# Kernel optimization log

Measured on AMD Instinct MI355X. Metric: run time of the kernel, lower is better.

The kernel has to match this reference:

```python
import jax, jax.numpy as jnp
import numpy as np

B, N, D = 4, 1024, 32      # clouds, points per cloud, feature dim
NW = 4                     # n_weights
THRESHOLD = 0.5
J = 3                      # wavelet scales (as in forward: J = 3)


def setup_inputs() -> dict:
    key = jax.random.key(0)
    k1, k2 = jax.random.split(key)
    point_clouds = jax.random.normal(k1, (B, N, D), dtype=jnp.float32)
    alphas = jax.random.uniform(k2, (NW, D), dtype=jnp.float32)
    sigma = jnp.float32(50.0)
    return {"point_clouds": point_clouds, "alphas": alphas, "sigma": sigma}


def reference(point_clouds, alphas, sigma):
    # X_nodes = pc * alpha_w for every (cloud p, weight w): [B, NW, N, D]
    X = point_clouds[:, None, :, :] * alphas[None, :, None, :]
    # compute_dist: ||xi||^2 + ||xj||^2 - 2 <xi, xj>  -> [B, NW, N, N]
    sq = jnp.sum(X * X, axis=-1)
    G = jnp.einsum('bwnd,bwmd->bwnm', X, X)
    Dm = sq[..., :, None] + sq[..., None, :] - 2.0 * G
    K = jnp.exp(-Dm / sigma)
    # threshold graph: keep kernel weight where K >= threshold (self-loops kept, K_ii = 1)
    A = (K >= THRESHOLD).astype(X.dtype)
    Wm = K * A
    deg = jnp.sum(Wm, axis=-1)  # >= 1 via self-loop
    # lazy random-walk diffusion operator P = 0.5 (I + D^{-1} W)
    P = 0.5 * (jnp.eye(N, dtype=X.dtype) + Wm / deg[..., None])
    # dyadic powers P^(2^j), j = 0..J
    powers = [P]
    for _ in range(J):
        powers.append(jnp.einsum('bwnm,bwmk->bwnk', powers[-1], powers[-1]))

    def apply(M, F):
        return jnp.einsum('bwnm,bwmd->bwnd', M, F)

    # first-order scattering |psi_j X| with psi_j = P^(2^(j)) - P^(2^(j+1))
    first = [jnp.abs(apply(powers[j] - powers[j + 1], X)) for j in range(J)]
    # second-order |psi_k |psi_j X|| for j < k
    second = [jnp.abs(apply(powers[k] - powers[k + 1], first[j]))
              for j in range(J) for k in range(j + 1, J)]
    feats = jnp.concatenate([X] + first + second, axis=-1)  # [B, NW, N, F0]
    pooled = jnp.mean(feats, axis=2)                        # mean pooling -> [B, NW, F0]
    # final view(B_pc, features * n_weights)
    return pooled.reshape(B, -1)
```

## Files before the change

### kernel.cpp

```cpp
#include <hip/hip_runtime.h>
#include <math.h>

#define NPTS 1024
#define DIM 32
#define NPAIR 16

typedef __attribute__((ext_vector_type(8))) short short8;
typedef __attribute__((ext_vector_type(4))) float f32x4;
typedef __attribute__((ext_vector_type(8))) unsigned short ushort8v;
typedef unsigned short u16;
typedef unsigned char u8;


__device__ __forceinline__ u16 bf16_rne(float v) {
    unsigned u = __float_as_uint(v);
    return (u16)((u + 0x7fffu + ((u >> 16) & 1u)) >> 16);
}
__device__ __forceinline__ float bf16_to_f32(u16 b) {
    return __uint_as_float(((unsigned)b) << 16);
}

__device__ __forceinline__ short8 unpack_w8(unsigned lo, unsigned hi) {
    short8 r;
#pragma unroll
    for (int j = 0; j < 4; j++) {
        float f0 = (float)((lo >> (8 * j)) & 0xffu);
        float f1 = (float)((hi >> (8 * j)) & 0xffu);
        r[j]     = (short)(__float_as_uint(f0) >> 16);
        r[j + 4] = (short)(__float_as_uint(f1) >> 16);
    }
    return r;
}

__global__ __launch_bounds__(256) void build_X(const float* __restrict__ pc,
                                               const float* __restrict__ alphas,
                                               float* __restrict__ X,
                                               float* __restrict__ sqX,
                                               float* __restrict__ deg,
                                               u16* __restrict__ hiT,
                                               u16* __restrict__ loT,
                                               float* __restrict__ poolP) {
    __shared__ float S[DIM][68];
    int pair = blockIdx.y, n0 = blockIdx.x * 64, tid = threadIdx.x;
    int b = pair >> 2, w = pair & 3;
    for (int e = tid; e < 512; e += 256) {
        int e4 = e * 4;
        int dn = e4 >> 5, dq = e4 & 31;
        float4 p = *(const float4*)&pc[((size_t)b * NPTS + n0 + dn) * DIM + dq];
        float4 al = *(const float4*)&alphas[w * DIM + dq];
        float4 x = make_float4(p.x * al.x, p.y * al.y, p.z * al.z, p.w * al.w);
        *(float4*)&X[((size_t)pair * NPTS + n0 + dn) * DIM + dq] = x;
        S[dq][dn] = x.x; S[dq + 1][dn] = x.y; S[dq + 2][dn] = x.z; S[dq + 3][dn] = x.w;
    }
    __syncthreads();
    if (tid < 64) {
        float s = 0.f;
#pragma unroll
        for (int d = 0; d < DIM; d++) { float v = S[d][tid]; s += v * v; }
        sqX[pair * NPTS + n0 + tid] = s;
        deg[pair * NPTS + n0 + tid] = 0.0f;
    }
    if (tid < 64) {
        int h = tid >> 5, d = tid & 31;
        float s = 0.f;
#pragma unroll
        for (int k = 0; k < 32; k++) s += S[d][h * 32 + k];
        poolP[(((size_t)0 * NPAIR + pair) * 32 + 2 * blockIdx.x + h) * 32 + d] = s;
    }
    for (int idx = tid; idx < DIM * 4; idx += 256) {
        int row = idx >> 2, nq = (idx & 3) * 16;
        ushort8v hv[2], lv[2];
#pragma unroll
        for (int i = 0; i < 16; i++) {
            float v = S[row][nq + i];
            u16 hb = bf16_rne(v);
            hv[i >> 3][i & 7] = hb;
            lv[i >> 3][i & 7] = bf16_rne(v - bf16_to_f32(hb));
        }
        int c0 = n0 + nq;
        int kt = c0 >> 5;
        int q0 = (c0 >> 3) & 3;
        int mm = row & 15;
        size_t base = ((((size_t)pair * 2 + (row >> 4)) * 32 + kt) << 9);
        *(ushort8v*)(hiT + base + (size_t)(q0 * 16 + mm) * 8)       = hv[0];
        *(ushort8v*)(hiT + base + (size_t)((q0 + 1) * 16 + mm) * 8) = hv[1];
        *(ushort8v*)(loT + base + (size_t)(q0 * 16 + mm) * 8)       = lv[0];
        *(ushort8v*)(loT + base + (size_t)((q0 + 1) * 16 + mm) * 8) = lv[1];
    }
}

__global__ __launch_bounds__(256, 4) void W_kernel(const float* __restrict__ X,
                                                   const float* __restrict__ sqX,
                                                   const float* __restrict__ sigp,
                                                   float* __restrict__ deg,
                                                   u8* __restrict__ W8) {
    int bid = blockIdx.x;
    int xcd = bid & 7, loc = bid >> 3;
    int pair = xcd * 2 + (loc & 1);
    int j0 = ((loc >> 1) & 3) * 256;
    int i0 = (loc >> 3) * 64;
    float rsig = -1.0f / (*sigp);
    const float* Xp = X + (size_t)pair * NPTS * DIM;

    __shared__ float XiT[DIM][68];
    __shared__ float XjT[DIM][68];
    __shared__ float sqjS[64];

    int tid = threadIdx.x;
    int cx = tid & 15, ry = tid >> 4;

    {
        int r = tid & 63, dgb = (tid >> 6) * 4;
#pragma unroll
        for (int p = 0; p < 2; p++) {
            int dg = dgb + p * 16;
            float4 v = *(const float4*)&Xp[(size_t)(i0 + r) * DIM + dg];
            XiT[dg][r] = v.x; XiT[dg + 1][r] = v.y; XiT[dg + 2][r] = v.z; XiT[dg + 3][r] = v.w;
        }
    }
    float sqi[4];
#pragma unroll
    for (int a = 0; a < 4; a++) sqi[a] = sqX[pair * NPTS + i0 + ry * 4 + a];

    float rs[4] = {0.f, 0.f, 0.f, 0.f};
#pragma unroll 1
    for (int jt = 0; jt < 256; jt += 64) {
        __syncthreads();
        {
            int r = tid & 63, dgb = (tid >> 6) * 4;
#pragma unroll
            for (int p = 0; p < 2; p++) {
                int dg = dgb + p * 16;
                float4 v = *(const float4*)&Xp[(size_t)(j0 + jt + r) * DIM + dg];
                XjT[dg][r] = v.x; XjT[dg + 1][r] = v.y; XjT[dg + 2][r] = v.z; XjT[dg + 3][r] = v.w;
            }
        }
        if (tid < 64) sqjS[tid] = sqX[pair * NPTS + j0 + jt + tid];
        __syncthreads();

        float dot[4][4] = {};
#pragma unroll
        for (int d = 0; d < DIM; d++) {
            float4 a = *(const float4*)&XiT[d][ry * 4];
            float4 b = *(const float4*)&XjT[d][cx * 4];
            dot[0][0] += a.x * b.x; dot[0][1] += a.x * b.y; dot[0][2] += a.x * b.z; dot[0][3] += a.x * b.w;
            dot[1][0] += a.y * b.x; dot[1][1] += a.y * b.y; dot[1][2] += a.y * b.z; dot[1][3] += a.y * b.w;
            dot[2][0] += a.z * b.x; dot[2][1] += a.z * b.y; dot[2][2] += a.z * b.z; dot[2][3] += a.z * b.w;
            dot[3][0] += a.w * b.x; dot[3][1] += a.w * b.y; dot[3][2] += a.w * b.z; dot[3][3] += a.w * b.w;
        }
#pragma unroll
        for (int a = 0; a < 4; a++) {
            int i = i0 + ry * 4 + a;
            int jb = j0 + jt + cx * 4;
            unsigned qw = 0;
#pragma unroll
            for (int bb = 0; bb < 4; bb++) {
                float Dm = sqi[a] + sqjS[cx * 4 + bb] - 2.0f * dot[a][bb];
                float K = __expf(Dm * rsig);
                float Wv = (K >= 0.5f) ? K : 0.0f;
                unsigned q = (unsigned)fmaf(Wv, 255.0f, 0.5f);
                rs[a] += (float)q;
                qw |= q << (8 * bb);
            }
            int kt = jb >> 5;
            int quad = (jb >> 3) & 3;
            int jj = jb & 7;
            size_t o = ((((size_t)pair * 64 + (i >> 4)) * 32 + kt) << 9)
                     + (size_t)(quad * 16 + (i & 15)) * 8 + jj;
            *(unsigned*)(W8 + o) = qw;
        }
    }
#pragma unroll
    for (int a = 0; a < 4; a++) {
        float s = rs[a];
        s += __shfl_xor(s, 1); s += __shfl_xor(s, 2);
        s += __shfl_xor(s, 4); s += __shfl_xor(s, 8);
        if (cx == 0) atomicAdd(&deg[pair * NPTS + i0 + ry * 4 + a], s);
    }
}

template <int DC>
__global__ __launch_bounds__(512, 4) void apply_fused(const u8* __restrict__ W8,
                                                      const u16* __restrict__ Yhi,
                                                      const u16* __restrict__ Ylo,
                                                      const float* __restrict__ deg,
                                                      const float* __restrict__ prevF,
                                                      int prevStride, int prevOff,
                                                      float* __restrict__ dstF,
                                                      int dstStride, int dstOff,
                                                      float* __restrict__ sliceF,
                                                      u16* __restrict__ hiT, u16* __restrict__ loT,
                                                      int tC0, int tCN) {
    constexpr int NT = DC / 16;
    constexpr int SP = DC + 4;
    __shared__ float S[4][32][SP];
    __shared__ float rdegS[32];
    int bid = blockIdx.x;
    int pair = (bid & 7) * 2 + ((bid >> 3) & 1);
    int r0 = (bid >> 4) * 32;
    int tid = threadIdx.x;
    int wv = tid >> 6, lane = tid & 63;
    int m = lane & 15, quad = lane >> 4;

    if (tid < 32) rdegS[tid] = 0.5f / deg[pair * NPTS + r0 + tid];

    int rt0 = (bid >> 4) * 2;
    const u8*  Wb  = W8  + ((((size_t)pair * 64 + rt0) * 32 + wv * 4) << 9) + (size_t)lane * 8;
    const u16* Ybh = Yhi + (((size_t)pair * NT * 32 + wv * 4) << 9) + (size_t)lane * 8;
    const u16* Ybl = Ylo + (((size_t)pair * NT * 32 + wv * 4) << 9) + (size_t)lane * 8;

    f32x4 acc[2][NT];
#pragma unroll
    for (int mt = 0; mt < 2; mt++)
#pragma unroll
        for (int nt = 0; nt < NT; nt++)
#pragma unroll
            for (int i = 0; i < 4; i++) acc[mt][nt][i] = 0.0f;

#pragma unroll 2
    for (int c = 0; c < 4; c++) {
        uint2 a0q = *(const uint2*)(Wb + ((size_t)c << 9));
        uint2 a1q = *(const uint2*)(Wb + ((size_t)(32 + c) << 9));
        short8 a0h = unpack_w8(a0q.x, a0q.y);
        short8 a1h = unpack_w8(a1q.x, a1q.y);
#pragma unroll
        for (int nt = 0; nt < NT; nt++) {
            short8 bh = *(const short8*)(Ybh + ((size_t)(nt * 32 + c) << 9));
            short8 bl = *(const short8*)(Ybl + ((size_t)(nt * 32 + c) << 9));
            acc[0][nt] = __builtin_amdgcn_mfma_f32_16x16x32_bf16(a0h, bh, acc[0][nt], 0, 0, 0);
            acc[0][nt] = __builtin_amdgcn_mfma_f32_16x16x32_bf16(a0h, bl, acc[0][nt], 0, 0, 0);
            acc[1][nt] = __builtin_amdgcn_mfma_f32_16x16x32_bf16(a1h, bh, acc[1][nt], 0, 0, 0);
            acc[1][nt] = __builtin_amdgcn_mfma_f32_16x16x32_bf16(a1h, bl, acc[1][nt], 0, 0, 0);
        }
    }

    if (wv < 4) {
#pragma unroll
        for (int mt = 0; mt < 2; mt++)
#pragma unroll
            for (int nt = 0; nt < NT; nt++)
#pragma unroll
                for (int i = 0; i < 4; i++)
                    S[wv][mt * 16 + quad * 4 + i][nt * 16 + m] = acc[mt][nt][i];
    }
    __syncthreads();
    if (wv >= 4) {
#pragma unroll
        for (int mt = 0; mt < 2; mt++)
#pragma unroll
            for (int nt = 0; nt < NT; nt++)
#pragma unroll
                for (int i = 0; i < 4; i++)
                    S[wv - 4][mt * 16 + quad * 4 + i][nt * 16 + m] += acc[mt][nt][i];
    }
    __syncthreads();

    constexpr int E2 = 32 * DC / 4;
    for (int e = tid; e < E2; e += 512) {
        int e4 = e * 4;
        int n = e4 / DC, d = e4 % DC;
        float4 s0 = *(const float4*)&S[0][n][d];
        float4 s1 = *(const float4*)&S[1][n][d];
        float4 s2 = *(const float4*)&S[2][n][d];
        float4 s3 = *(const float4*)&S[3][n][d];
        float4 pv = *(const float4*)&prevF[((size_t)pair * NPTS + r0 + n) * prevStride + prevOff + d];
        float r = rdegS[n];
        float4 o = make_float4(0.5f * pv.x + r * (s0.x + s1.x + s2.x + s3.x),
                               0.5f * pv.y + r * (s0.y + s1.y + s2.y + s3.y),
                               0.5f * pv.z + r * (s0.z + s1.z + s2.z + s3.z),
                               0.5f * pv.w + r * (s0.w + s1.w + s2.w + s3.w));
        *(float4*)&dstF[((size_t)pair * NPTS + r0 + n) * dstStride + dstOff + d] = o;
        if (sliceF && d >= 32 && d < 64)
            *(float4*)&sliceF[((size_t)pair * NPTS + r0 + n) * 32 + (d - 32)] = o;
        *(float4*)&S[0][n][d] = o;
    }
    __syncthreads();

    if (hiT) {
        int NFo = tCN >> 4;
        for (int e = tid; e < tCN * 4; e += 512) {
            int row = e >> 2, nq = (e & 3) * 8;
            ushort8v hv, lv;
#pragma unroll
            for (int j = 0; j < 8; j++) {
                float v = S[0][nq + j][tC0 + row];
                u16 hb = bf16_rne(v);
                hv[j] = hb;
                lv[j] = bf16_rne(v - bf16_to_f32(hb));
            }
            int c0 = r0 + nq;
            size_t o = ((((size_t)pair * NFo + (row >> 4)) * 32 + (c0 >> 5)) << 9)
                     + (size_t)((((c0 >> 3) & 3) * 16 + (row & 15))) * 8;
            *(ushort8v*)(hiT + o) = hv;
            *(ushort8v*)(loT + o) = lv;
        }
    }
}

template <int DC>
__global__ __launch_bounds__(512, 4) void apply_fused2(const u8* __restrict__ W8,
                                                       const u16* __restrict__ Yhi,
                                                       const u16* __restrict__ Ylo,
                                                       const float* __restrict__ deg,
                                                       const float* __restrict__ prevF,
                                                       int prevStride, int prevOff,
                                                       float* __restrict__ dstF,
                                                       int dstStride, int dstOff,
                                                       float* __restrict__ sliceF,
                                                       u16* __restrict__ hiT, u16* __restrict__ loT,
                                                       int tC0, int tCN) {
    constexpr int NF = DC / 16;
    constexpr int SP = 36;
    __shared__ float S[4][64][SP];
    __shared__ float rdegS[64];
    int bid = blockIdx.x;
    int pair = (bid & 7) * 2 + ((bid >> 3) & 1);
    int rseg = (bid >> 4) & 15;
    int ch = bid >> 8;
    int r0 = rseg * 64;
    int tid = threadIdx.x;
    int wv = tid >> 6, lane = tid & 63;
    int m = lane & 15, quad = lane >> 4;

    if (tid < 64) rdegS[tid] = 0.5f / deg[pair * NPTS + r0 + tid];

    const u8*  Wb  = W8  + ((((size_t)pair * 64 + rseg * 4) * 32 + wv * 4) << 9) + (size_t)lane * 8;
    const u16* Ybh = Yhi + ((((size_t)pair * NF + ch * 2) * 32 + wv * 4) << 9) + (size_t)lane * 8;
    const u16* Ybl = Ylo + ((((size_t)pair * NF + ch * 2) * 32 + wv * 4) << 9) + (size_t)lane * 8;

    f32x4 acc[4][2];
#pragma unroll
    for (int mt = 0; mt < 4; mt++)
#pragma unroll
        for (int nt = 0; nt < 2; nt++)
#pragma unroll
            for (int i = 0; i < 4; i++) acc[mt][nt][i] = 0.0f;

#pragma unroll 2
    for (int c = 0; c < 4; c++) {
        uint2 aq[4];
#pragma unroll
        for (int mt = 0; mt < 4; mt++)
            aq[mt] = *(const uint2*)(Wb + ((size_t)(mt * 32 + c) << 9));
        short8 a[4];
#pragma unroll
        for (int mt = 0; mt < 4; mt++) a[mt] = unpack_w8(aq[mt].x, aq[mt].y);
#pragma unroll
        for (int nt = 0; nt < 2; nt++) {
            short8 bh = *(const short8*)(Ybh + ((size_t)(nt * 32 + c) << 9));
            short8 bl = *(const short8*)(Ybl + ((size_t)(nt * 32 + c) << 9));
#pragma unroll
            for (int mt = 0; mt < 4; mt++) {
                acc[mt][nt] = __builtin_amdgcn_mfma_f32_16x16x32_bf16(a[mt], bh, acc[mt][nt], 0, 0, 0);
                acc[mt][nt] = __builtin_amdgcn_mfma_f32_16x16x32_bf16(a[mt], bl, acc[mt][nt], 0, 0, 0);
            }
        }
    }

    if (wv < 4) {
#pragma unroll
        for (int mt = 0; mt < 4; mt++)
#pragma unroll
            for (int nt = 0; nt < 2; nt++)
#pragma unroll
                for (int i = 0; i < 4; i++)
                    S[wv][mt * 16 + quad * 4 + i][nt * 16 + m] = acc[mt][nt][i];
    }
    __syncthreads();
    if (wv >= 4) {
#pragma unroll
        for (int mt = 0; mt < 4; mt++)
#pragma unroll
            for (int nt = 0; nt < 2; nt++)
#pragma unroll
                for (int i = 0; i < 4; i++)
                    S[wv - 4][mt * 16 + quad * 4 + i][nt * 16 + m] += acc[mt][nt][i];
    }
    __syncthreads();

    {
        int n = tid >> 3, d = (tid & 7) * 4;
        int col = ch * 32 + d;
        float4 s0 = *(const float4*)&S[0][n][d];
        float4 s1 = *(const float4*)&S[1][n][d];
        float4 s2 = *(const float4*)&S[2][n][d];
        float4 s3 = *(const float4*)&S[3][n][d];
        float4 pv = *(const float4*)&prevF[((size_t)pair * NPTS + r0 + n) * prevStride + prevOff + col];
        float r = rdegS[n];
        float4 o = make_float4(0.5f * pv.x + r * (s0.x + s1.x + s2.x + s3.x),
                               0.5f * pv.y + r * (s0.y + s1.y + s2.y + s3.y),
                               0.5f * pv.z + r * (s0.z + s1.z + s2.z + s3.z),
                               0.5f * pv.w + r * (s0.w + s1.w + s2.w + s3.w));
        *(float4*)&dstF[((size_t)pair * NPTS + r0 + n) * dstStride + dstOff + col] = o;
        if (sliceF && ch == 1)
            *(float4*)&sliceF[((size_t)pair * NPTS + r0 + n) * 32 + d] = o;
        *(float4*)&S[0][n][d] = o;
    }
    __syncthreads();

    int gr0 = 32 * ch - tC0;
    if (hiT && gr0 >= 0 && gr0 < tCN) {
        int NFo = tCN >> 4;
        if (tid < 256) {
            int lr = tid >> 3, nq = (tid & 7) * 8;
            ushort8v hv, lv;
#pragma unroll
            for (int j = 0; j < 8; j++) {
                float v = S[0][nq + j][lr];
                u16 hb = bf16_rne(v);
                hv[j] = hb;
                lv[j] = bf16_rne(v - bf16_to_f32(hb));
            }
            int gr = gr0 + lr;
            int c0 = r0 + nq;
            size_t o = ((((size_t)pair * NFo + (gr >> 4)) * 32 + (c0 >> 5)) << 9)
                     + (size_t)((((c0 >> 3) & 3) * 16 + (gr & 15))) * 8;
            *(ushort8v*)(hiT + o) = hv;
            *(ushort8v*)(loT + o) = lv;
        }
    }
}

__global__ __launch_bounds__(512, 4) void apply_fused_m0(const u8* __restrict__ W8,
                                                         const u16* __restrict__ Yhi,
                                                         const u16* __restrict__ Ylo,
                                                         const float* __restrict__ deg,
                                                         const float* __restrict__ prevF,
                                                         const float* __restrict__ A1,
                                                         const float* __restrict__ A2,
                                                         float* __restrict__ M0,
                                                         u16* __restrict__ hiT, u16* __restrict__ loT,
                                                         float* __restrict__ poolP) {
    constexpr int DC = 32, NT = 2, SP = 36;
    __shared__ float S[4][32][SP];
    __shared__ float rdegS[32];
    __shared__ float SB[96][33];
    int bid = blockIdx.x;
    int pair = (bid & 7) * 2 + ((bid >> 3) & 1);
    int r0 = (bid >> 4) * 32;
    int rt = bid >> 4;
    int tid = threadIdx.x;
    int wv = tid >> 6, lane = tid & 63;
    int m = lane & 15, quad = lane >> 4;

    if (tid < 32) rdegS[tid] = 0.5f / deg[pair * NPTS + r0 + tid];

    int rt0 = rt * 2;
    const u8*  Wb  = W8  + ((((size_t)pair * 64 + rt0) * 32 + wv * 4) << 9) + (size_t)lane * 8;
    const u16* Ybh = Yhi + (((size_t)pair * NT * 32 + wv * 4) << 9) + (size_t)lane * 8;
    const u16* Ybl = Ylo + (((size_t)pair * NT * 32 + wv * 4) << 9) + (size_t)lane * 8;

    f32x4 acc[2][NT];
#pragma unroll
    for (int mt = 0; mt < 2; mt++)
#pragma unroll
        for (int nt = 0; nt < NT; nt++)
#pragma unroll
            for (int i = 0; i < 4; i++) acc[mt][nt][i] = 0.0f;

#pragma unroll 2
    for (int c = 0; c < 4; c++) {
        uint2 a0q = *(const uint2*)(Wb + ((size_t)c << 9));
        uint2 a1q = *(const uint2*)(Wb + ((size_t)(32 + c) << 9));
        short8 a0h = unpack_w8(a0q.x, a0q.y);
        short8 a1h = unpack_w8(a1q.x, a1q.y);
#pragma unroll
        for (int nt = 0; nt < NT; nt++) {
            short8 bh = *(const short8*)(Ybh + ((size_t)(nt * 32 + c) << 9));
            short8 bl = *(const short8*)(Ybl + ((size_t)(nt * 32 + c) << 9));
            acc[0][nt] = __builtin_amdgcn_mfma_f32_16x16x32_bf16(a0h, bh, acc[0][nt], 0, 0, 0);
            acc[0][nt] = __builtin_amdgcn_mfma_f32_16x16x32_bf16(a0h, bl, acc[0][nt], 0, 0, 0);
            acc[1][nt] = __builtin_amdgcn_mfma_f32_16x16x32_bf16(a1h, bh, acc[1][nt], 0, 0, 0);
            acc[1][nt] = __builtin_amdgcn_mfma_f32_16x16x32_bf16(a1h, bl, acc[1][nt], 0, 0, 0);
        }
    }

    if (wv < 4) {
#pragma unroll
        for (int mt = 0; mt < 2; mt++)
#pragma unroll
            for (int nt = 0; nt < NT; nt++)
#pragma unroll
                for (int i = 0; i < 4; i++)
                    S[wv][mt * 16 + quad * 4 + i][nt * 16 + m] = acc[mt][nt][i];
    }
    __syncthreads();
    if (wv >= 4) {
#pragma unroll
        for (int mt = 0; mt < 2; mt++)
#pragma unroll
            for (int nt = 0; nt < NT; nt++)
#pragma unroll
                for (int i = 0; i < 4; i++)
                    S[wv - 4][mt * 16 + quad * 4 + i][nt * 16 + m] += acc[mt][nt][i];
    }
    __syncthreads();

    for (int e = tid; e < 256; e += 512) {
        int e4 = e * 4;
        int n = e4 / DC, d = e4 % DC;
        float4 s0 = *(const float4*)&S[0][n][d];
        float4 s1 = *(const float4*)&S[1][n][d];
        float4 s2 = *(const float4*)&S[2][n][d];
        float4 s3 = *(const float4*)&S[3][n][d];
        float4 pv = *(const float4*)&prevF[((size_t)pair * NPTS + r0 + n) * 32 + d];
        float r = rdegS[n];
        float4 o = make_float4(0.5f * pv.x + r * (s0.x + s1.x + s2.x + s3.x),
                               0.5f * pv.y + r * (s0.y + s1.y + s2.y + s3.y),
                               0.5f * pv.z + r * (s0.z + s1.z + s2.z + s3.z),
                               0.5f * pv.w + r * (s0.w + s1.w + s2.w + s3.w));
        *(float4*)&M0[((size_t)pair * NPTS + r0 + n) * 96 + d] = o;
        *(float4*)&S[0][n][d] = o;
    }
    __syncthreads();

    if (tid < 256) {
        int dn = tid >> 3, dq = (tid & 7) * 4;
        size_t pn = (size_t)pair * NPTS + r0 + dn;
        float4 a1 = *(const float4*)&A1[pn * 32 + dq];
        float4 a2 = *(const float4*)&A2[pn * 32 + dq];
        float4 t4 = *(const float4*)&S[0][dn][dq];
        float4 f0 = make_float4(fabsf(a1.x - a2.x), fabsf(a1.y - a2.y), fabsf(a1.z - a2.z), fabsf(a1.w - a2.w));
        float4 f1 = make_float4(fabsf(a2.x - t4.x), fabsf(a2.y - t4.y), fabsf(a2.z - t4.z), fabsf(a2.w - t4.w));
        *(float4*)&M0[pn * 96 + 32 + dq] = f0;
        *(float4*)&M0[pn * 96 + 64 + dq] = f1;
        SB[dq][dn] = t4.x; SB[dq + 1][dn] = t4.y; SB[dq + 2][dn] = t4.z; SB[dq + 3][dn] = t4.w;
        SB[32 + dq][dn] = f0.x; SB[33 + dq][dn] = f0.y; SB[34 + dq][dn] = f0.z; SB[35 + dq][dn] = f0.w;
        SB[64 + dq][dn] = f1.x; SB[65 + dq][dn] = f1.y; SB[66 + dq][dn] = f1.z; SB[67 + dq][dn] = f1.w;
    }
    __syncthreads();

    if (tid < 64) {
        int gg = tid >> 5, d = tid & 31;
        float s = 0.f;
#pragma unroll
        for (int k = 0; k < 32; k++) s += SB[32 + gg * 32 + d][k];
        poolP[(((size_t)(1 + gg) * NPAIR + pair) * 32 + rt) * 32 + d] = s;
    }

    for (int e = tid; e < 96 * 4; e += 512) {
        int row = e >> 2, nq = (e & 3) * 8;
        ushort8v hv, lv;
#pragma unroll
        for (int j = 0; j < 8; j++) {
            float v = SB[row][nq + j];
            u16 hb = bf16_rne(v);
            hv[j] = hb;
            lv[j] = bf16_rne(v - bf16_to_f32(hb));
        }
        int c0 = r0 + nq;
        size_t o = ((((size_t)pair * 6 + (row >> 4)) * 32 + (c0 >> 5)) << 9)
                 + (size_t)((((c0 >> 3) & 3) * 16 + (row & 15))) * 8;
        *(ushort8v*)(hiT + o) = hv;
        *(ushort8v*)(loT + o) = lv;
    }
}

__global__ __launch_bounds__(512, 4) void apply_fused_pool2(const u8* __restrict__ W8,
                                                            const u16* __restrict__ Yhi,
                                                            const u16* __restrict__ Ylo,
                                                            const float* __restrict__ deg,
                                                            const float* __restrict__ prevF,
                                                            float* __restrict__ Z8,
                                                            const float* __restrict__ M0,
                                                            const float* __restrict__ M2p,
                                                            const float* __restrict__ M4f,
                                                            float* __restrict__ poolP) {
    constexpr int NF = 4, SP = 36;
    __shared__ float S[4][64][SP];
    __shared__ float rdegS[64];
    int bid = blockIdx.x;
    int pair = (bid & 7) * 2 + ((bid >> 3) & 1);
    int rseg = (bid >> 4) & 15;
    int ch = bid >> 8;
    int r0 = rseg * 64;
    int tid = threadIdx.x;
    int wv = tid >> 6, lane = tid & 63;
    int m = lane & 15, quad = lane >> 4;

    if (tid < 64) rdegS[tid] = 0.5f / deg[pair * NPTS + r0 + tid];

    const u8*  Wb  = W8  + ((((size_t)pair * 64 + rseg * 4) * 32 + wv * 4) << 9) + (size_t)lane * 8;
    const u16* Ybh = Yhi + ((((size_t)pair * NF + ch * 2) * 32 + wv * 4) << 9) + (size_t)lane * 8;
    const u16* Ybl = Ylo + ((((size_t)pair * NF + ch * 2) * 32 + wv * 4) << 9) + (size_t)lane * 8;

    f32x4 acc[4][2];
#pragma unroll
    for (int mt = 0; mt < 4; mt++)
#pragma unroll
        for (int nt = 0; nt < 2; nt++)
#pragma unroll
            for (int i = 0; i < 4; i++) acc[mt][nt][i] = 0.0f;

#pragma unroll 2
    for (int c = 0; c < 4; c++) {
        uint2 aq[4];
#pragma unroll
        for (int mt = 0; mt < 4; mt++)
            aq[mt] = *(const uint2*)(Wb + ((size_t)(mt * 32 + c) << 9));
        short8 a[4];
#pragma unroll
        for (int mt = 0; mt < 4; mt++) a[mt] = unpack_w8(aq[mt].x, aq[mt].y);
#pragma unroll
        for (int nt = 0; nt < 2; nt++) {
            short8 bh = *(const short8*)(Ybh + ((size_t)(nt * 32 + c) << 9));
            short8 bl = *(const short8*)(Ybl + ((size_t)(nt * 32 + c) << 9));
#pragma unroll
            for (int mt = 0; mt < 4; mt++) {
                acc[mt][nt] = __builtin_amdgcn_mfma_f32_16x16x32_bf16(a[mt], bh, acc[mt][nt], 0, 0, 0);
                acc[mt][nt] = __builtin_amdgcn_mfma_f32_16x16x32_bf16(a[mt], bl, acc[mt][nt], 0, 0, 0);
            }
        }
    }

    if (wv < 4) {
#pragma unroll
        for (int mt = 0; mt < 4; mt++)
#pragma unroll
            for (int nt = 0; nt < 2; nt++)
#pragma unroll
                for (int i = 0; i < 4; i++)
                    S[wv][mt * 16 + quad * 4 + i][nt * 16 + m] = acc[mt][nt][i];
    }
    __syncthreads();
    if (wv >= 4) {
#pragma unroll
        for (int mt = 0; mt < 4; mt++)
#pragma unroll
            for (int nt = 0; nt < 2; nt++)
#pragma unroll
                for (int i = 0; i < 4; i++)
                    S[wv - 4][mt * 16 + quad * 4 + i][nt * 16 + m] += acc[mt][nt][i];
    }
    __syncthreads();

    {
        int n = tid >> 3, d = (tid & 7) * 4;
        int col = ch * 32 + d;
        float4 s0 = *(const float4*)&S[0][n][d];
        float4 s1 = *(const float4*)&S[1][n][d];
        float4 s2 = *(const float4*)&S[2][n][d];
        float4 s3 = *(const float4*)&S[3][n][d];
        float4 pv = *(const float4*)&prevF[((size_t)pair * NPTS + r0 + n) * 64 + col];
        float r = rdegS[n];
        float4 o = make_float4(0.5f * pv.x + r * (s0.x + s1.x + s2.x + s3.x),
                               0.5f * pv.y + r * (s0.y + s1.y + s2.y + s3.y),
                               0.5f * pv.z + r * (s0.z + s1.z + s2.z + s3.z),
                               0.5f * pv.w + r * (s0.w + s1.w + s2.w + s3.w));
        *(float4*)&Z8[((size_t)pair * NPTS + r0 + n) * 64 + col] = o;
        *(float4*)&S[0][n][d] = o;
    }
    __syncthreads();

    if (ch == 0) {
        if (tid < 192) {
            int gsel = tid >> 6, h = (tid >> 5) & 1, d = tid & 31;
            float s = 0.f;
#pragma unroll 4
            for (int k = 0; k < 32; k++) {
                int n = h * 32 + k;
                size_t pn = (size_t)pair * NPTS + r0 + n;
                float v;
                switch (gsel) {
                    case 0: v = fabsf(M0[pn * 96 + d] - M4f[pn * 96 + d]); break;
                    case 1: v = fabsf(M2p[pn * 32 + d] - M4f[pn * 96 + 32 + d]); break;
                    default: v = fabsf(M4f[pn * 96 + 32 + d] - S[0][n][d]); break;
                }
                s += v;
            }
            poolP[(((size_t)(3 + gsel) * NPAIR + pair) * 32 + 2 * rseg + h) * 32 + d] = s;
        }
    } else {
        if (tid < 64) {
            int h = tid >> 5, d = tid & 31;
            float s = 0.f;
#pragma unroll 4
            for (int k = 0; k < 32; k++) {
                int n = h * 32 + k;
                size_t pn = (size_t)pair * NPTS + r0 + n;
                s += fabsf(M4f[pn * 96 + 64 + d] - S[0][n][d]);
            }
            poolP[(((size_t)6 * NPAIR + pair) * 32 + 2 * rseg + h) * 32 + d] = s;
        }
    }
}

__global__ __launch_bounds__(256) void pool_final(const float* __restrict__ partial,
                                                  float* __restrict__ out) {
    int pair = blockIdx.x;
    int t = threadIdx.x;
    if (t < 224) {
        int g = t >> 5, d = t & 31;
        float s = 0.0f;
#pragma unroll 8
        for (int r = 0; r < 32; r++)
            s += partial[(((size_t)g * NPAIR + pair) * 32 + r) * 32 + d];
        out[(size_t)pair * 224 + t] = s * (1.0f / 1024.0f);
    }
}

extern "C" void kernel_launch(void* const* d_in, const int* in_sizes, int n_in,
                              void* d_out, int out_size, void* d_ws, size_t ws_size,
                              hipStream_t stream) {
    const float* pc     = (const float*)d_in[0];
    const float* alphas = (const float*)d_in[1];
    const float* sigp   = (const float*)d_in[2];
    float* out = (float*)d_out;
    float* ws = (float*)d_ws;

    float* X    = ws;
    float* sqX  = X + 524288;
    float* deg  = sqX + 16384;
    u8* W8 = (u8*)(deg + 16384);
    float* A1   = (float*)(W8 + 16777216);
    float* A2   = A1 + 524288;
    u16* T32a_h = (u16*)(A2 + 524288);
    u16* T32a_l = T32a_h + 524288;
    u16* T32b_h = T32a_l + 524288;
    u16* T32b_l = T32b_h + 524288;
    float* F96b = A1;
    float* M0   = (float*)(T32b_l + 524288);
    float* M2p  = M0 + 1572864;
    float* M4f  = M2p + 524288;
    float* Z8   = M4f + 1572864;
    float* F96a = Z8 + 1048576;
    float* A3   = F96a;
    u16* T96a_h = (u16*)(F96a + 1572864);
    u16* T96a_l = T96a_h + 1572864;
    u16* T96b_h = T96a_l + 1572864;
    u16* T96b_l = T96b_h + 1572864;
    u16* T64a_h = T96a_h;
    u16* T64a_l = T96a_l;
    u16* T64b_h = T96b_h;
    u16* T64b_l = T96b_l;
    float* poolP = (float*)(T96b_l + 1572864);

    dim3 b256(256), b512(512);

    build_X<<<dim3(16, NPAIR), b256, 0, stream>>>(pc, alphas, X, sqX, deg, T32a_h, T32a_l, poolP);
    W_kernel<<<dim3(1024), b256, 0, stream>>>(X, sqX, sigp, deg, W8);

    apply_fused<32><<<dim3(512), b512, 0, stream>>>(W8, T32a_h, T32a_l, deg,
                                             X, 32, 0, A1, 32, 0, nullptr, T32b_h, T32b_l, 0, 32);
    apply_fused<32><<<dim3(512), b512, 0, stream>>>(W8, T32b_h, T32b_l, deg,
                                             A1, 32, 0, A2, 32, 0, nullptr, T32a_h, T32a_l, 0, 32);
    apply_fused<32><<<dim3(512), b512, 0, stream>>>(W8, T32a_h, T32a_l, deg,
                                             A2, 32, 0, A3, 32, 0, nullptr, T32b_h, T32b_l, 0, 32);
    apply_fused_m0<<<dim3(512), b512, 0, stream>>>(W8, T32b_h, T32b_l, deg,
                                             A3, A1, A2, M0, T96a_h, T96a_l, poolP);

    apply_fused2<96><<<dim3(768), b512, 0, stream>>>(W8, T96a_h, T96a_l, deg,
                                             M0, 96, 0, F96a, 96, 0, nullptr, T96b_h, T96b_l, 0, 96);
    apply_fused2<96><<<dim3(768), b512, 0, stream>>>(W8, T96b_h, T96b_l, deg,
                                             F96a, 96, 0, F96b, 96, 0, M2p, T96a_h, T96a_l, 0, 96);
    apply_fused2<96><<<dim3(768), b512, 0, stream>>>(W8, T96a_h, T96a_l, deg,
                                             F96b, 96, 0, F96a, 96, 0, nullptr, T96b_h, T96b_l, 0, 96);
    apply_fused2<96><<<dim3(768), b512, 0, stream>>>(W8, T96b_h, T96b_l, deg,
                                             F96a, 96, 0, M4f, 96, 0, nullptr, T64a_h, T64a_l, 32, 64);

    apply_fused2<64><<<dim3(512), b512, 0, stream>>>(W8, T64a_h, T64a_l, deg,
                                             M4f, 96, 32, F96a, 64, 0, nullptr, T64b_h, T64b_l, 0, 64);
    apply_fused2<64><<<dim3(512), b512, 0, stream>>>(W8, T64b_h, T64b_l, deg,
                                             F96a, 64, 0, F96b, 64, 0, nullptr, T64a_h, T64a_l, 0, 64);
    apply_fused2<64><<<dim3(512), b512, 0, stream>>>(W8, T64a_h, T64a_l, deg,
                                             F96b, 64, 0, F96a, 64, 0, nullptr, T64b_h, T64b_l, 0, 64);
    apply_fused_pool2<<<dim3(512), b512, 0, stream>>>(W8, T64b_h, T64b_l, deg,
                                             F96a, Z8, M0, M2p, M4f, poolP);

    pool_final<<<dim3(NPAIR), b256, 0, stream>>>(poolP, out);
}
```

Baseline: 224.5 us.

## Compute kernel-matrix Gram products with split-bf16 MFMA instead of scalar FP32

The W-matrix kernel now computes pairwise dot products with three bf16 MFMA instructions on hi/lo split operands, replacing the scalar FP32 loop over transposed shared-memory tiles. build_X also emits bf16 hi/lo copies of X so the MFMA kernel can load its fragments directly. Quantized weights are staged in shared memory and written out as 8-byte vectors, and per-row degree sums are taken from that tile. This aims to cut the ALU cost of the Gram step. The split-bf16 product drops the lo*lo term, which slightly changes precision near the threshold, and build_X now does extra conversion work and stores.

```diff
diff --git a/kernel.cpp b/kernel.cpp
--- a/kernel.cpp
+++ b/kernel.cpp
@@ -8,6 +8,7 @@
 typedef __attribute__((ext_vector_type(8))) short short8;
 typedef __attribute__((ext_vector_type(4))) float f32x4;
 typedef __attribute__((ext_vector_type(8))) unsigned short ushort8v;
+typedef __attribute__((ext_vector_type(4))) unsigned short ushort4v;
 typedef unsigned short u16;
 typedef unsigned char u8;
 
@@ -35,6 +36,8 @@
 __global__ __launch_bounds__(256) void build_X(const float* __restrict__ pc,
                                                const float* __restrict__ alphas,
                                                float* __restrict__ X,
+                                               u16* __restrict__ Xbh,
+                                               u16* __restrict__ Xbl,
                                                float* __restrict__ sqX,
                                                float* __restrict__ deg,
                                                u16* __restrict__ hiT,
@@ -49,7 +52,18 @@
         float4 p = *(const float4*)&pc[((size_t)b * NPTS + n0 + dn) * DIM + dq];
         float4 al = *(const float4*)&alphas[w * DIM + dq];
         float4 x = make_float4(p.x * al.x, p.y * al.y, p.z * al.z, p.w * al.w);
-        *(float4*)&X[((size_t)pair * NPTS + n0 + dn) * DIM + dq] = x;
+        size_t ro = ((size_t)pair * NPTS + n0 + dn) * DIM + dq;
+        *(float4*)&X[ro] = x;
+        ushort4v xh, xl;
+        float xv[4] = {x.x, x.y, x.z, x.w};
+#pragma unroll
+        for (int j = 0; j < 4; j++) {
+            u16 hb = bf16_rne(xv[j]);
+            xh[j] = hb;
+            xl[j] = bf16_rne(xv[j] - bf16_to_f32(hb));
+        }
+        *(ushort4v*)(Xbh + ro) = xh;
+        *(ushort4v*)(Xbl + ro) = xl;
         S[dq][dn] = x.x; S[dq + 1][dn] = x.y; S[dq + 2][dn] = x.z; S[dq + 3][dn] = x.w;
     }
     __syncthreads();
@@ -89,93 +103,80 @@
     }
 }
 
-__global__ __launch_bounds__(256, 4) void W_kernel(const float* __restrict__ X,
-                                                   const float* __restrict__ sqX,
-                                                   const float* __restrict__ sigp,
-                                                   float* __restrict__ deg,
-                                                   u8* __restrict__ W8) {
+__global__ __launch_bounds__(512, 4) void W_mfma(const u16* __restrict__ Xbh,
+                                                 const u16* __restrict__ Xbl,
+                                                 const float* __restrict__ sqX,
+                                                 const float* __restrict__ sigp,
+                                                 float* __restrict__ deg,
+                                                 u8* __restrict__ W8) {
+    __shared__ __align__(16) u8 S8[64][264];
+    __shared__ float sqiS[64];
+    __shared__ float sqjS[256];
     int bid = blockIdx.x;
     int xcd = bid & 7, loc = bid >> 3;
     int pair = xcd * 2 + (loc & 1);
-    int j0 = ((loc >> 1) & 3) * 256;
-    int i0 = (loc >> 3) * 64;
+    int rest = loc >> 1;
+    int i0 = (rest & 15) * 64;
+    int j0 = (rest >> 4) * 256;
     float rsig = -1.0f / (*sigp);
-    const float* Xp = X + (size_t)pair * NPTS * DIM;
-
-    __shared__ float XiT[DIM][68];
-    __shared__ float XjT[DIM][68];
-    __shared__ float sqjS[64];
-
     int tid = threadIdx.x;
-    int cx = tid & 15, ry = tid >> 4;
+    int wv = tid >> 6, lane = tid & 63;
+    int m = lane & 15, quad = lane >> 4;
+
+    if (tid < 64) sqiS[tid] = sqX[pair * NPTS + i0 + tid];
+    if (tid < 256) sqjS[tid] = sqX[pair * NPTS + j0 + tid];
+
+    int ibl = (wv & 3) * 16;
+    int jh = (wv >> 2) * 128;
+    size_t axy = ((size_t)pair * NPTS + i0 + ibl + m) * DIM + quad * 8;
+    short8 Ah = *(const short8*)(Xbh + axy);
+    short8 Al = *(const short8*)(Xbl + axy);
+    float sqi[4];
+    __syncthreads();
+#pragma unroll
+    for (int ii = 0; ii < 4; ii++) sqi[ii] = sqiS[ibl + quad * 4 + ii];
+
+#pragma unroll
+    for (int jt = 0; jt < 8; jt++) {
+        int jbl = jh + jt * 16;
+        size_t bxy = ((size_t)pair * NPTS + j0 + jbl + m) * DIM + quad * 8;
+        short8 Bh = *(const short8*)(Xbh + bxy);
+        short8 Bl = *(const short8*)(Xbl + bxy);
+        f32x4 g = {0.f, 0.f, 0.f, 0.f};
+        g = __builtin_amdgcn_mfma_f32_16x16x32_bf16(Ah, Bh, g, 0, 0, 0);
+        g = __builtin_amdgcn_mfma_f32_16x16x32_bf16(Ah, Bl, g, 0, 0, 0);
+        g = __builtin_amdgcn_mfma_f32_16x16x32_bf16(Al, Bh, g, 0, 0, 0);
+        float sqj = sqjS[jbl + m];
+#pragma unroll
+        for (int ii = 0; ii < 4; ii++) {
+            float Dm = sqi[ii] + sqj - 2.0f * g[ii];
+            float K = __expf(Dm * rsig);
+            float Wv = (K >= 0.5f) ? K : 0.0f;
+            unsigned q = (unsigned)fmaf(Wv, 255.0f, 0.5f);
+            S8[ibl + quad * 4 + ii][jbl + m] = (u8)q;
+        }
+    }
+    __syncthreads();
 
     {
-        int r = tid & 63, dgb = (tid >> 6) * 4;
-#pragma unroll
-        for (int p = 0; p < 2; p++) {
-            int dg = dgb + p * 16;
-            float4 v = *(const float4*)&Xp[(size_t)(i0 + r) * DIM + dg];
-            XiT[dg][r] = v.x; XiT[dg + 1][r] = v.y; XiT[dg + 2][r] = v.z; XiT[dg + 3][r] = v.w;
-        }
-    }
-    float sqi[4];
-#pragma unroll
-    for (int a = 0; a < 4; a++) sqi[a] = sqX[pair * NPTS + i0 + ry * 4 + a];
-
-    float rs[4] = {0.f, 0.f, 0.f, 0.f};
-#pragma unroll 1
-    for (int jt = 0; jt < 256; jt += 64) {
-        __syncthreads();
-        {
-            int r = tid & 63, dgb = (tid >> 6) * 4;
-#pragma unroll
-            for (int p = 0; p < 2; p++) {
-                int dg = dgb + p * 16;
-                float4 v = *(const float4*)&Xp[(size_t)(j0 + jt + r) * DIM + dg];
-                XjT[dg][r] = v.x; XjT[dg + 1][r] = v.y; XjT[dg + 2][r] = v.z; XjT[dg + 3][r] = v.w;
-            }
-        }
-        if (tid < 64) sqjS[tid] = sqX[pair * NPTS + j0 + jt + tid];
-        __syncthreads();
-
-        float dot[4][4] = {};
-#pragma unroll
-        for (int d = 0; d < DIM; d++) {
-            float4 a = *(const float4*)&XiT[d][ry * 4];
-            float4 b = *(const float4*)&XjT[d][cx * 4];
-            dot[0][0] += a.x * b.x; dot[0][1] += a.x * b.y; dot[0][2] += a.x * b.z; dot[0][3] += a.x * b.w;
-            dot[1][0] += a.y * b.x; dot[1][1] += a.y * b.y; dot[1][2] += a.y * b.z; dot[1][3] += a.y * b.w;
-            dot[2][0] += a.z * b.x; dot[2][1] += a.z * b.y; dot[2][2] += a.z * b.z; dot[2][3] += a.z * b.w;
-            dot[3][0] += a.w * b.x; dot[3][1] += a.w * b.y; dot[3][2] += a.w * b.z; dot[3][3] += a.w * b.w;
-        }
-#pragma unroll
-        for (int a = 0; a < 4; a++) {
-            int i = i0 + ry * 4 + a;
-            int jb = j0 + jt + cx * 4;
-            unsigned qw = 0;
-#pragma unroll
-            for (int bb = 0; bb < 4; bb++) {
-                float Dm = sqi[a] + sqjS[cx * 4 + bb] - 2.0f * dot[a][bb];
-                float K = __expf(Dm * rsig);
-                float Wv = (K >= 0.5f) ? K : 0.0f;
-                unsigned q = (unsigned)fmaf(Wv, 255.0f, 0.5f);
-                rs[a] += (float)q;
-                qw |= q << (8 * bb);
-            }
-            int kt = jb >> 5;
-            int quad = (jb >> 3) & 3;
-            int jj = jb & 7;
-            size_t o = ((((size_t)pair * 64 + (i >> 4)) * 32 + kt) << 9)
-                     + (size_t)(quad * 16 + (i & 15)) * 8 + jj;
-            *(unsigned*)(W8 + o) = qw;
-        }
-    }
-#pragma unroll
-    for (int a = 0; a < 4; a++) {
-        float s = rs[a];
-        s += __shfl_xor(s, 1); s += __shfl_xor(s, 2);
-        s += __shfl_xor(s, 4); s += __shfl_xor(s, 8);
-        if (cx == 0) atomicAdd(&deg[pair * NPTS + i0 + ry * 4 + a], s);
+        int i = tid >> 3, t = tid & 7;
+        int iglob = i0 + i;
+        size_t wbase = (((size_t)pair * 64 + (iglob >> 4)) * 32) << 9;
+        int si = 0;
+#pragma unroll
+        for (int k = 0; k < 4; k++) {
+            int j8 = t * 32 + k * 8;
+            uint2 w = *(const uint2*)&S8[i][j8];
+            si += (int)((w.x & 0xffu) + ((w.x >> 8) & 0xffu) + ((w.x >> 16) & 0xffu) + (w.x >> 24)
+                      + (w.y & 0xffu) + ((w.y >> 8) & 0xffu) + ((w.y >> 16) & 0xffu) + (w.y >> 24));
+            int jg = j0 + j8;
+            size_t o = wbase + ((size_t)(jg >> 5) << 9)
+                     + (size_t)(((jg >> 3) & 3) * 16 + (iglob & 15)) * 8;
+            *(uint2*)(W8 + o) = w;
+        }
+        float s = (float)si;
+        s += __shfl_xor(s, 1); s += __shfl_xor(s, 2); s += __shfl_xor(s, 4);
+        if (t == 0) atomicAdd(&deg[pair * NPTS + iglob], s);
     }
 }
 
@@ -734,11 +735,13 @@
     u16* T64b_h = T96b_h;
     u16* T64b_l = T96b_l;
     float* poolP = (float*)(T96b_l + 1572864);
+    u16* Xbh = (u16*)(poolP + 114688);
+    u16* Xbl = Xbh + 524288;
 
     dim3 b256(256), b512(512);
 
-    build_X<<<dim3(16, NPAIR), b256, 0, stream>>>(pc, alphas, X, sqX, deg, T32a_h, T32a_l, poolP);
-    W_kernel<<<dim3(1024), b256, 0, stream>>>(X, sqX, sigp, deg, W8);
+    build_X<<<dim3(16, NPAIR), b256, 0, stream>>>(pc, alphas, X, Xbh, Xbl, sqX, deg, T32a_h, T32a_l, poolP);
+    W_mfma<<<dim3(1024), b512, 0, stream>>>(Xbh, Xbl, sqX, sigp, deg, W8);
 
     apply_fused<32><<<dim3(512), b512, 0, stream>>>(W8, T32a_h, T32a_l, deg,
                                              X, 32, 0, A1, 32, 0, nullptr, T32b_h, T32b_l, 0, 32);
```

Measured after the change: 213.7 us (median of 2 runs). 4.8% less time.
